# Kernel tuning notes

Measured on AMD Instinct MI355X. Metric: run time of the kernel, lower is better.

## Reference

```python
import math
import jax, jax.numpy as jnp
import numpy as np

N_NODES = 200000          # len(tree)
HIDDEN = 1024             # args.hidden_dim
SINGLE_DIM = HIDDEN // 2  # lower/upper halves of the circle embedding
TREE_HEIGHT = 8           # path length (root-to-leaf)
BATCH = 2048              # positive pairs per step
N_NEG = 8                 # args.negative_sample_size
CIRCLE_MARGIN = 1.0       # args.circle_margin
SCR = 2.0 * math.pi       # single_circle_range


def setup_inputs() -> dict:
    key = jax.random.key(0)
    k1, k2, k3 = jax.random.split(key, 3)
    node_embedding = jax.random.normal(k1, (N_NODES, HIDDEN), dtype=jnp.float32)
    pos_path = jax.random.randint(k2, (BATCH, 2, TREE_HEIGHT), 0, N_NODES, dtype=jnp.int32)
    neg_path = jax.random.randint(k3, (BATCH, N_NEG, TREE_HEIGHT), 0, N_NODES, dtype=jnp.int32)
    return {"node_embedding": node_embedding, "pos_path": pos_path, "neg_path": neg_path}


def _inter_size(p1, p2):
    # |set(path1) & set(path2)| assuming distinct ids within a path.
    # p1: [..., P], p2: [..., P] -> [...]
    return (p1[..., :, None] == p2[..., None, :]).any(-1).sum(-1)


def _calc_dist(emb, p1, p2, diff):
    # emb: [V, H]; p1, p2: [..., P] int; diff: [...] float
    d = emb[p1] - emb[p2]                       # [..., P, H]
    low, high = d[..., :SINGLE_DIM], d[..., SINGLE_DIM:]
    dist = (0.5 * (low + high)).sum(-2)         # [..., SINGLE_DIM]
    return dist + (diff - 1.0)[..., None] * SCR


def reference(node_embedding, pos_path, neg_path):
    p1 = pos_path[:, 0]                          # [B, P]
    p2 = pos_path[:, 1]                          # [B, P]
    # calc_dist clamps diff to >= 1; calc_diff (used for k) does NOT.
    diff_pos = jnp.maximum(TREE_HEIGHT - _inter_size(p1, p2), 1).astype(jnp.float32)
    pos_dist = _calc_dist(node_embedding, p1, p2, diff_pos)          # [B, SD]

    diff_neg_raw = (TREE_HEIGHT - _inter_size(p1[:, None, :], neg_path)).astype(jnp.float32)  # [B, N]
    k = diff_neg_raw - 1.0                                            # unclamped, per source
    diff_neg = jnp.maximum(diff_neg_raw, 1.0)
    neg_dist = _calc_dist(node_embedding, p1[:, None, :], neg_path, diff_neg)  # [B, N, SD]

    tmp = k[..., None] * CIRCLE_MARGIN * SCR + pos_dist[:, None, :] - neg_dist  # [B, N, SD]
    tmp_p = jnp.maximum(tmp, 0.0)
    punish = jnp.sqrt((tmp_p * tmp_p).sum(-1)).sum()   # sum of per-(b,n) L2 norms
    return punish.reshape(1)
```

## Files before the change

kernel.cpp:

```cpp
#include <hip/hip_runtime.h>

constexpr int   TH    = 8;
constexpr int   NNEG  = 8;
constexpr int   HID4  = 256;
constexpr int   HALF4 = 128;
constexpr float SCR_F = 6.2831853071795864769f;

__global__ void zero_kernel(float* out) { out[0] = 0.0f; }

__global__ __launch_bounds__(128)
void punish_kernel(const float* __restrict__ emb,
                   const int*   __restrict__ pos_path,
                   const int*   __restrict__ neg_path,
                   float*       __restrict__ out)
{
    const int b = blockIdx.x;
    const int t = threadIdx.x;

    __shared__ int   s_p1[TH];
    __shared__ int   s_p2[TH];
    __shared__ int   s_neg[NNEG * TH];
    __shared__ float s_C[NNEG];
    __shared__ float s_red[2][NNEG];

    if (t < TH) {
        s_p1[t] = pos_path[b * 2 * TH + t];
        s_p2[t] = pos_path[b * 2 * TH + TH + t];
    }
    if (t < NNEG * TH) {
        s_neg[t] = neg_path[b * NNEG * TH + t];
    }
    __syncthreads();

    if (t < NNEG) {
        int inter_pos = 0;
#pragma unroll
        for (int i = 0; i < TH; i++) {
            const int v = s_p1[i];
            bool f = false;
#pragma unroll
            for (int j = 0; j < TH; j++) f = f || (v == s_p2[j]);
            inter_pos += f ? 1 : 0;
        }
        const float diff_pos = fmaxf((float)(TH - inter_pos), 1.0f);

        const int n = t;
        int inter_n = 0;
#pragma unroll
        for (int i = 0; i < TH; i++) {
            const int v = s_p1[i];
            bool f = false;
#pragma unroll
            for (int j = 0; j < TH; j++) f = f || (v == s_neg[n * TH + j]);
            inter_n += f ? 1 : 0;
        }
        const int raw = TH - inter_n;
        s_C[n] = (diff_pos - 1.0f - (raw == 0 ? 1.0f : 0.0f)) * SCR_F;
    }
    __syncthreads();

    const float4* __restrict__ embv = (const float4*)emb;

    float4 sp2 = {0.f, 0.f, 0.f, 0.f};
#pragma unroll
    for (int h = 0; h < TH; h++) {
        const float4* row = embv + (long)s_p2[h] * HID4;
        const float4 lo = row[t];
        const float4 hi = row[HALF4 + t];
        sp2.x += lo.x + hi.x;
        sp2.y += lo.y + hi.y;
        sp2.z += lo.z + hi.z;
        sp2.w += lo.w + hi.w;
    }

    float a[NNEG];
#pragma unroll
    for (int n = 0; n < NNEG; n++) {
        float4 sn = {0.f, 0.f, 0.f, 0.f};
#pragma unroll
        for (int h = 0; h < TH; h++) {
            const float4* row = embv + (long)s_neg[n * TH + h] * HID4;
            const float4 lo = row[t];
            const float4 hi = row[HALF4 + t];
            sn.x += lo.x + hi.x;
            sn.y += lo.y + hi.y;
            sn.z += lo.z + hi.z;
            sn.w += lo.w + hi.w;
        }
        const float c = s_C[n];
        float vx = c + 0.5f * (sn.x - sp2.x);
        float vy = c + 0.5f * (sn.y - sp2.y);
        float vz = c + 0.5f * (sn.z - sp2.z);
        float vw = c + 0.5f * (sn.w - sp2.w);
        vx = fmaxf(vx, 0.f); vy = fmaxf(vy, 0.f);
        vz = fmaxf(vz, 0.f); vw = fmaxf(vw, 0.f);
        a[n] = vx * vx + vy * vy + vz * vz + vw * vw;
    }

#pragma unroll
    for (int n = 0; n < NNEG; n++) {
#pragma unroll
        for (int off = 32; off > 0; off >>= 1) {
            a[n] += __shfl_down(a[n], off, 64);
        }
    }
    const int lane = t & 63;
    const int wid  = t >> 6;
    if (lane == 0) {
#pragma unroll
        for (int n = 0; n < NNEG; n++) s_red[wid][n] = a[n];
    }
    __syncthreads();

    if (t == 0) {
        float total = 0.f;
#pragma unroll
        for (int n = 0; n < NNEG; n++) {
            total += sqrtf(s_red[0][n] + s_red[1][n]);
        }
        atomicAdd(out, total);
    }
}

extern "C" void kernel_launch(void* const* d_in, const int* in_sizes, int n_in,
                              void* d_out, int out_size, void* d_ws, size_t ws_size,
                              hipStream_t stream) {
    const float* emb      = (const float*)d_in[0];
    const int*   pos_path = (const int*)d_in[1];
    const int*   neg_path = (const int*)d_in[2];
    float*       out      = (float*)d_out;

    const int BATCH = in_sizes[1] / (2 * TH);

    zero_kernel<<<1, 1, 0, stream>>>(out);
    punish_kernel<<<BATCH, 128, 0, stream>>>(emb, pos_path, neg_path, out);
}
```

Measured before the change: 962.3 us.

## Split punish kernel into prep, per-negative gather, and final reduce kernels

Result: no change. 977.7 us (+1.6%).

```diff
diff --git a/kernel.cpp b/kernel.cpp
--- a/kernel.cpp
+++ b/kernel.cpp
@@ -6,29 +6,22 @@
 constexpr int   HALF4 = 128;
 constexpr float SCR_F = 6.2831853071795864769f;
 
-__global__ void zero_kernel(float* out) { out[0] = 0.0f; }
-
 __global__ __launch_bounds__(128)
-void punish_kernel(const float* __restrict__ emb,
-                   const int*   __restrict__ pos_path,
-                   const int*   __restrict__ neg_path,
-                   float*       __restrict__ out)
+void prep_kernel(const float* __restrict__ emb,
+                 const int*   __restrict__ pos_path,
+                 const int*   __restrict__ neg_path,
+                 float*       __restrict__ sp2_out,
+                 float*       __restrict__ C_out)
 {
     const int b = blockIdx.x;
     const int t = threadIdx.x;
 
-    __shared__ int   s_p1[TH];
-    __shared__ int   s_p2[TH];
-    __shared__ int   s_neg[NNEG * TH];
-    __shared__ float s_C[NNEG];
-    __shared__ float s_red[2][NNEG];
+    __shared__ int s_p1[TH];
+    __shared__ int s_p2[TH];
 
     if (t < TH) {
         s_p1[t] = pos_path[b * 2 * TH + t];
         s_p2[t] = pos_path[b * 2 * TH + TH + t];
-    }
-    if (t < NNEG * TH) {
-        s_neg[t] = neg_path[b * NNEG * TH + t];
     }
     __syncthreads();
 
@@ -45,22 +38,25 @@
         const float diff_pos = fmaxf((float)(TH - inter_pos), 1.0f);
 
         const int n = t;
+        int negj[TH];
+#pragma unroll
+        for (int j = 0; j < TH; j++)
+            negj[j] = neg_path[(b * NNEG + n) * TH + j];
+
         int inter_n = 0;
 #pragma unroll
         for (int i = 0; i < TH; i++) {
             const int v = s_p1[i];
             bool f = false;
 #pragma unroll
-            for (int j = 0; j < TH; j++) f = f || (v == s_neg[n * TH + j]);
+            for (int j = 0; j < TH; j++) f = f || (v == negj[j]);
             inter_n += f ? 1 : 0;
         }
         const int raw = TH - inter_n;
-        s_C[n] = (diff_pos - 1.0f - (raw == 0 ? 1.0f : 0.0f)) * SCR_F;
+        C_out[b * NNEG + n] = (diff_pos - 1.0f - (raw == 0 ? 1.0f : 0.0f)) * SCR_F;
     }
-    __syncthreads();
 
     const float4* __restrict__ embv = (const float4*)emb;
-
     float4 sp2 = {0.f, 0.f, 0.f, 0.f};
 #pragma unroll
     for (int h = 0; h < TH; h++) {
@@ -72,54 +68,78 @@
         sp2.z += lo.z + hi.z;
         sp2.w += lo.w + hi.w;
     }
+    ((float4*)sp2_out)[(long)b * HALF4 + t] = sp2;
+}
 
-    float a[NNEG];
+__global__ __launch_bounds__(128)
+void neg_kernel(const float* __restrict__ emb,
+                const int*   __restrict__ neg_path,
+                const float* __restrict__ sp2_in,
+                const float* __restrict__ C_in,
+                float*       __restrict__ partial,
+                int batch)
+{
+    const int bn = blockIdx.x;
+    const int b  = bn % batch;
+    const int n  = bn / batch;
+    const int t  = threadIdx.x;
+    const int idx = b * NNEG + n;
+
+    const int* __restrict__ neg = neg_path + (long)idx * TH;
+    const float c = C_in[idx];
+
+    const float4* __restrict__ embv = (const float4*)emb;
+    float4 sn = {0.f, 0.f, 0.f, 0.f};
 #pragma unroll
-    for (int n = 0; n < NNEG; n++) {
-        float4 sn = {0.f, 0.f, 0.f, 0.f};
-#pragma unroll
-        for (int h = 0; h < TH; h++) {
-            const float4* row = embv + (long)s_neg[n * TH + h] * HID4;
-            const float4 lo = row[t];
-            const float4 hi = row[HALF4 + t];
-            sn.x += lo.x + hi.x;
-            sn.y += lo.y + hi.y;
-            sn.z += lo.z + hi.z;
-            sn.w += lo.w + hi.w;
-        }
-        const float c = s_C[n];
-        float vx = c + 0.5f * (sn.x - sp2.x);
-        float vy = c + 0.5f * (sn.y - sp2.y);
-        float vz = c + 0.5f * (sn.z - sp2.z);
-        float vw = c + 0.5f * (sn.w - sp2.w);
-        vx = fmaxf(vx, 0.f); vy = fmaxf(vy, 0.f);
-        vz = fmaxf(vz, 0.f); vw = fmaxf(vw, 0.f);
-        a[n] = vx * vx + vy * vy + vz * vz + vw * vw;
+    for (int h = 0; h < TH; h++) {
+        const float4* row = embv + (long)neg[h] * HID4;
+        const float4 lo = row[t];
+        const float4 hi = row[HALF4 + t];
+        sn.x += lo.x + hi.x;
+        sn.y += lo.y + hi.y;
+        sn.z += lo.z + hi.z;
+        sn.w += lo.w + hi.w;
     }
 
+    const float4 sp2 = ((const float4*)sp2_in)[(long)b * HALF4 + t];
+    float vx = c + 0.5f * (sn.x - sp2.x);
+    float vy = c + 0.5f * (sn.y - sp2.y);
+    float vz = c + 0.5f * (sn.z - sp2.z);
+    float vw = c + 0.5f * (sn.w - sp2.w);
+    vx = fmaxf(vx, 0.f); vy = fmaxf(vy, 0.f);
+    vz = fmaxf(vz, 0.f); vw = fmaxf(vw, 0.f);
+    float a = vx * vx + vy * vy + vz * vz + vw * vw;
+
 #pragma unroll
-    for (int n = 0; n < NNEG; n++) {
-#pragma unroll
-        for (int off = 32; off > 0; off >>= 1) {
-            a[n] += __shfl_down(a[n], off, 64);
-        }
+    for (int off = 32; off > 0; off >>= 1) {
+        a += __shfl_down(a, off, 64);
     }
+    __shared__ float s_red[2];
     const int lane = t & 63;
     const int wid  = t >> 6;
-    if (lane == 0) {
+    if (lane == 0) s_red[wid] = a;
+    __syncthreads();
+    if (t == 0) partial[idx] = sqrtf(s_red[0] + s_red[1]);
+}
+
+__global__ __launch_bounds__(256)
+void reduce_kernel(const float* __restrict__ partial, int nval,
+                   float* __restrict__ out)
+{
+    const int t = threadIdx.x;
+    float s = 0.f;
+    for (int i = t; i < nval; i += 256) s += partial[i];
+
 #pragma unroll
-        for (int n = 0; n < NNEG; n++) s_red[wid][n] = a[n];
+    for (int off = 32; off > 0; off >>= 1) {
+        s += __shfl_down(s, off, 64);
     }
+    __shared__ float s_red[4];
+    const int lane = t & 63;
+    const int wid  = t >> 6;
+    if (lane == 0) s_red[wid] = s;
     __syncthreads();
-
-    if (t == 0) {
-        float total = 0.f;
-#pragma unroll
-        for (int n = 0; n < NNEG; n++) {
-            total += sqrtf(s_red[0][n] + s_red[1][n]);
-        }
-        atomicAdd(out, total);
-    }
+    if (t == 0) out[0] = s_red[0] + s_red[1] + s_red[2] + s_red[3];
 }
 
 extern "C" void kernel_launch(void* const* d_in, const int* in_sizes, int n_in,
@@ -132,6 +152,12 @@
 
     const int BATCH = in_sizes[1] / (2 * TH);
 
-    zero_kernel<<<1, 1, 0, stream>>>(out);
-    punish_kernel<<<BATCH, 128, 0, stream>>>(emb, pos_path, neg_path, out);
+    float* sp2     = (float*)d_ws;
+    float* Cb      = sp2 + (size_t)BATCH * 512;
+    float* partial = Cb  + (size_t)BATCH * NNEG;
+
+    prep_kernel<<<BATCH, 128, 0, stream>>>(emb, pos_path, neg_path, sp2, Cb);
+    neg_kernel<<<BATCH * NNEG, 128, 0, stream>>>(emb, neg_path, sp2, Cb,
+                                                 partial, BATCH);
+    reduce_kernel<<<1, 256, 0, stream>>>(partial, BATCH * NNEG, out);
 }
```
